# Kernel optimization log

Measured on AMD Instinct MI355X. Metric: run time of the kernel, lower is better.

## Reference

```python
import jax, jax.numpy as jnp
import numpy as np

NEG_SLOPE = 0.01  # torch F.leaky_relu default


def setup_inputs() -> dict:
    key = jax.random.key(0)
    k1, k2, k3, k4 = jax.random.split(key, 4)
    N, E, R, D = 100000, 1250000, 16, 64
    ego_embed = jax.random.normal(k1, (N, D), dtype=jnp.float32) * 0.1
    relation_weights = jax.random.normal(k2, (R, D, D), dtype=jnp.float32) * (1.0 / np.sqrt(D))
    edge_index = jax.random.randint(k3, (2, E), 0, N, dtype=jnp.int32)
    edge_type = jax.random.randint(k4, (E,), 0, R, dtype=jnp.int32)
    return {"ego_embed": ego_embed, "relation_weights": relation_weights,
            "edge_index": edge_index, "edge_type": edge_type}


def reference(ego_embed, relation_weights, edge_index, edge_type):
    head, tail = edge_index[0], edge_index[1]
    n_entities = ego_embed.shape[0]
    # Transform every node by every relation once ([R,N,D]) instead of
    # materializing the per-edge [E,D,D] weight gather the torch bmm implies;
    # same math: transformed_head[e] = ego_embed[head[e]] @ W[edge_type[e]].
    transformed_all = jnp.einsum('nd,rdk->rnk', ego_embed, relation_weights)
    transformed_head = transformed_all[edge_type, head]        # [E, D]
    tail_emb = ego_embed[tail]                                  # [E, D]
    scores = jax.nn.leaky_relu(jnp.sum(transformed_head * tail_emb, axis=1),
                               negative_slope=NEG_SLOPE)        # [E]
    exp_scores = jnp.exp(scores)                                # unnormalized attention
    denom = jax.ops.segment_sum(exp_scores, head, num_segments=n_entities)[head]
    norm_att = exp_scores / denom                               # segment softmax
    weighted = tail_emb * norm_att[:, None]                     # [E, D]
    # scatter_mean: segment sum / per-segment edge count (clamped to 1)
    summed = jax.ops.segment_sum(weighted, head, num_segments=n_entities)
    counts = jax.ops.segment_sum(jnp.ones_like(exp_scores), head, num_segments=n_entities)
    return summed / jnp.maximum(counts, 1.0)[:, None]
```

## Files before the change

kernel.cpp:

```cpp
#include <hip/hip_runtime.h>
#include <stdint.h>

#define NEG_SLOPE 0.01f
#define HPG 32
#define TSTR 72
#define BSH 5
#define NBMX 3200
#define K1CH 16384
#define CAP3 1024

typedef float f32x4 __attribute__((ext_vector_type(4)));
typedef short short8 __attribute__((ext_vector_type(8)));
typedef unsigned int u32;

#define DPPADD(v, ctrl) ((v) + __int_as_float(__builtin_amdgcn_update_dpp( \
        0, __float_as_int(v), (ctrl), 0xF, 0xF, true)))

__device__ inline short f2bf(float f) {
    union { float f; uint32_t u; } x; x.f = f;
    uint32_t r = x.u + 0x7FFF + ((x.u >> 16) & 1);
    return (short)(r >> 16);
}
__device__ inline float bf2f(unsigned short u) {
    union { uint32_t u; float f; } x; x.u = ((uint32_t)u) << 16; return x.f;
}

__global__ void __launch_bounds__(512) kA(
        const int* __restrict__ head, const int* __restrict__ tail,
        const int* __restrict__ etype, int E, int NB, int nblk,
        u32* __restrict__ staging, int* bucket_cur,
        const float* __restrict__ ego, unsigned short* __restrict__ ego_bf,
        int NE8, const float* __restrict__ rw, short* __restrict__ wfrag) {
    int t = threadIdx.x;
    int bid = blockIdx.x;
    if (bid < nblk) {
        __shared__ int lcnt[NBMX], lbase[NBMX], lfill[NBMX];
        for (int b = t; b < NBMX; b += 512) lcnt[b] = 0;
        __syncthreads();
        long long base = (long long)bid * K1CH;
        #pragma unroll
        for (int s = 0; s < K1CH / 512; ++s) {
            long long e = base + t + s * 512;
            if (e < E) atomicAdd(&lcnt[head[e] >> BSH], 1);
        }
        __syncthreads();
        for (int b = t; b < NB; b += 512) {
            int c = lcnt[b];
            lbase[b] = c ? atomicAdd(&bucket_cur[b], c) : 0;
            lfill[b] = 0;
        }
        __syncthreads();
        #pragma unroll
        for (int s = 0; s < K1CH / 512; ++s) {
            long long e = base + t + s * 512;
            if (e < E) {
                int h = head[e];
                int bk = h >> BSH;
                int rk = atomicAdd(&lfill[bk], 1);
                int pos = lbase[bk] + rk;
                if (pos >= CAP3) pos = CAP3 - 1;
                staging[(size_t)bk * CAP3 + pos] =
                    (u32)tail[e] | ((u32)etype[e] << 20) | ((u32)(h & 31) << 24);
            }
        }
    } else {
        int ib = bid - nblk;
        if (ib < 16) {
            int r = ib;
            int lane = t & 63;
            int c = lane & 15, q = lane >> 4;
            int pair = t >> 6;
            int t4 = pair >> 1, kh = pair & 1;
            int m = t4 * 16 + c;
            short8 f;
            for (int j = 0; j < 8; ++j) {
                int k = kh * 32 + q * 8 + j;
                f[j] = f2bf(rw[r * 4096 + k * 64 + m]);
            }
            *(short8*)(wfrag + ((size_t)((r * 4 + t4) * 2 + kh) * 64 + lane) * 8) = f;
        }
        int i = ib * 512 + t;
        if (i < NE8) {
            const float4* p = (const float4*)ego + (size_t)i * 2;
            float4 a = p[0], b = p[1];
            short8 v;
            v[0] = f2bf(a.x); v[1] = f2bf(a.y); v[2] = f2bf(a.z); v[3] = f2bf(a.w);
            v[4] = f2bf(b.x); v[5] = f2bf(b.y); v[6] = f2bf(b.z); v[7] = f2bf(b.w);
            *(short8*)(ego_bf + (size_t)i * 8) = v;
        }
    }
}

__global__ void __launch_bounds__(512, 4) k4_fused(
        const unsigned short* __restrict__ ego_bf,
        const short* __restrict__ wfrag,
        const u32* __restrict__ staging,
        const int* __restrict__ bucket_cur,
        float* __restrict__ out, int N) {
    __shared__ unsigned short T[16 * HPG * TSTR];
    __shared__ u32 lrec[CAP3];
    __shared__ int lhc[HPG], lofs[HPG], lcn[HPG];
    int tid = threadIdx.x;
    int wave = tid >> 6;
    int lane = tid & 63;
    int c = lane & 15, q = lane >> 4;
    int b = blockIdx.x;
    int hb = b * HPG;

    if (tid < HPG) lhc[tid] = 0;
    __syncthreads();
    int cnt_raw = bucket_cur[b];
    int cntb = cnt_raw > CAP3 ? CAP3 : cnt_raw;
    const u32* sb = staging + (size_t)b * CAP3;
    u32 r0 = 0, r1 = 0; int rk0 = -1, rk1 = -1;
    if (tid < cntb)       { r0 = sb[tid];       rk0 = atomicAdd(&lhc[r0 >> 24], 1); }
    if (tid + 512 < cntb) { r1 = sb[tid + 512]; rk1 = atomicAdd(&lhc[r1 >> 24], 1); }
    __syncthreads();
    if (tid < 64) {
        int v = (lane < HPG) ? lhc[lane] : 0;
        int inc = v;
        for (int off = 1; off < HPG; off <<= 1) {
            int u = __shfl_up(inc, off);
            if (lane >= off) inc += u;
        }
        if (lane < HPG) { lofs[lane] = inc - v; lcn[lane] = v; }
    }
    __syncthreads();
    if (rk0 >= 0) lrec[lofs[r0 >> 24] + rk0] = r0;
    if (rk1 >= 0) lrec[lofs[r1 >> 24] + rk1] = r1;

    for (int t = 0; t < 2; ++t) {
        int r = wave * 2 + t;
        const short* wp = wfrag + (size_t)r * 4096;
        short8 wf[4][2];
        #pragma unroll
        for (int t4 = 0; t4 < 4; ++t4)
            #pragma unroll
            for (int kh = 0; kh < 2; ++kh)
                wf[t4][kh] = *(const short8*)(wp + ((size_t)((t4 * 2 + kh) * 64 + lane)) * 8);
        #pragma unroll
        for (int hf = 0; hf < 2; ++hf) {
            int hrow = hb + hf * 16 + c;
            if (hrow >= N) hrow = N - 1;
            const unsigned short* hr = ego_bf + (size_t)hrow * 64;
            short8 b0 = *(const short8*)(hr + q * 8);
            short8 b1 = *(const short8*)(hr + 32 + q * 8);
            #pragma unroll
            for (int t4 = 0; t4 < 4; ++t4) {
                f32x4 a = {0.f, 0.f, 0.f, 0.f};
                a = __builtin_amdgcn_mfma_f32_16x16x32_bf16(wf[t4][0], b0, a, 0, 0, 0);
                a = __builtin_amdgcn_mfma_f32_16x16x32_bf16(wf[t4][1], b1, a, 0, 0, 0);
                ushort4 us;
                us.x = (unsigned short)f2bf(a[0]);
                us.y = (unsigned short)f2bf(a[1]);
                us.z = (unsigned short)f2bf(a[2]);
                us.w = (unsigned short)f2bf(a[3]);
                *(ushort4*)&T[(size_t)(r * HPG + hf * 16 + c) * TSTR + t4 * 16 + q * 4] = us;
            }
        }
    }
    __syncthreads();

    int hql = wave * 4 + q;
    int h = hb + hql;
    if (h >= N) return;
    int lq = c;
    int g2 = lq >> 3, c8 = lq & 7;
    int s0 = lofs[hql];
    int cnt = lcn[hql];
    int nbt = (cnt + 15) >> 4;
    float acc[8] = {0.f, 0.f, 0.f, 0.f, 0.f, 0.f, 0.f, 0.f};
    float den = 0.f;

    auto recAt = [&](int b2, int j) -> u32 {
        int idx = b2 * 16 + j * 2 + g2;
        return (idx < cnt) ? lrec[s0 + idx] : 0;
    };

    u32 rjA[8]; short8 rowsA[8];
    #pragma unroll
    for (int j = 0; j < 8; ++j) rjA[j] = recAt(0, j);
    #pragma unroll
    for (int j = 0; j < 8; ++j)
        rowsA[j] = *(const short8*)(ego_bf + (size_t)(rjA[j] & 0xFFFFF) * 64 + c8 * 8);
    for (int b2 = 0; b2 < nbt; ++b2) {
        u32 rjB[8]; short8 rowsB[8];
        bool more = (b2 + 1 < nbt);
        if (more) {
            #pragma unroll
            for (int j = 0; j < 8; ++j) rjB[j] = recAt(b2 + 1, j);
            #pragma unroll
            for (int j = 0; j < 8; ++j)
                rowsB[j] = *(const short8*)(ego_bf + (size_t)(rjB[j] & 0xFFFFF) * 64 + c8 * 8);
        }
        int ng = cnt - b2 * 16; if (ng > 16) ng = 16;
        #pragma unroll
        for (int sIt = 0; sIt < 8; ++sIt) {
            if (sIt * 2 < ng) {
                int ty = (rjA[sIt] >> 20) & 15;
                short8 trw = *(const short8*)&T[(size_t)(ty * HPG + hql) * TSTR + c8 * 8];
                float rf[8];
                float sa = 0.f, sb2 = 0.f;
                #pragma unroll
                for (int k = 0; k < 4; ++k) {
                    rf[k] = bf2f((unsigned short)rowsA[sIt][k]);
                    sa += rf[k] * bf2f((unsigned short)trw[k]);
                }
                #pragma unroll
                for (int k = 4; k < 8; ++k) {
                    rf[k] = bf2f((unsigned short)rowsA[sIt][k]);
                    sb2 += rf[k] * bf2f((unsigned short)trw[k]);
                }
                float s = sa + sb2;
                s = DPPADD(s, 0xB1);
                s = DPPADD(s, 0x4E);
                s = DPPADD(s, 0x141);
                float lr = s > 0.f ? s : NEG_SLOPE * s;
                float w = (sIt * 2 + g2 < ng) ? __expf(lr) : 0.f;
                den += w;
                #pragma unroll
                for (int k = 0; k < 8; ++k) acc[k] += w * rf[k];
            }
        }
        if (more) {
            #pragma unroll
            for (int j = 0; j < 8; ++j) { rjA[j] = rjB[j]; rowsA[j] = rowsB[j]; }
        }
    }
    den = DPPADD(den, 0x128);
    #pragma unroll
    for (int k = 0; k < 8; ++k) acc[k] = DPPADD(acc[k], 0x128);
    if (g2 == 0) {
        float sc = (cnt > 0) ? 1.f / (den * (float)cnt) : 0.f;
        float4 v0 = {acc[0] * sc, acc[1] * sc, acc[2] * sc, acc[3] * sc};
        float4 v1 = {acc[4] * sc, acc[5] * sc, acc[6] * sc, acc[7] * sc};
        float* op = out + (size_t)h * 64 + c8 * 8;
        *(float4*)op = v0;
        *(float4*)(op + 4) = v1;
    }
}

extern "C" void kernel_launch(void* const* d_in, const int* in_sizes, int n_in,
                              void* d_out, int out_size, void* d_ws, size_t ws_size,
                              hipStream_t stream) {
    const float* ego = (const float*)d_in[0];
    const float* rw  = (const float*)d_in[1];
    const int* eidx  = (const int*)d_in[2];
    const int* etyp  = (const int*)d_in[3];
    int N = in_sizes[0] / 64;
    int E = in_sizes[3];
    const int* head = eidx;
    const int* tail = eidx + E;
    float* out = (float*)d_out;

    char* ws = (char*)d_ws;
    size_t o = 0;
    auto take = [&](size_t bytes) -> char* {
        char* p = ws + o;
        o = (o + bytes + 255) & ~(size_t)255;
        return p;
    };
    int NB = (N + HPG - 1) >> BSH;
    if (NB > NBMX) NB = NBMX;
    int nblk = (E + K1CH - 1) / K1CH;
    int NE8 = N * 8;
    int nbI = (NE8 + 511) / 512;
    if (nbI < 16) nbI = 16;
    unsigned short* ego_bf = (unsigned short*)take((size_t)N * 64 * 2);
    short* wfrag    = (short*)take(16 * 4096 * 2);
    u32* staging    = (u32*)take((size_t)NB * CAP3 * 4);
    int* bucket_cur = (int*)take((size_t)NBMX * 4);
    (void)ws_size; (void)n_in; (void)out_size;

    hipMemsetAsync(bucket_cur, 0, (size_t)NBMX * 4, stream);
    kA<<<nblk + nbI, 512, 0, stream>>>(head, tail, etyp, E, NB, nblk,
                                       staging, bucket_cur,
                                       ego, ego_bf, NE8, rw, wfrag);
    k4_fused<<<NB, 512, 0, stream>>>(ego_bf, wfrag, staging, bucket_cur,
                                     out, N);
}
```

Before: 196.6 us.

## Fuse all stages into one cooperative persistent kernel with grid syncs

Replaces the memset plus two-kernel pipeline with a single cooperative-launch persistent kernel of 512 blocks, separated by grid-wide syncs: bf16 conversion, edge binning, then per-tile attention aggregation. Binning now uses coarse 256-head buckets with 4096-edge chunks, and each tile re-scans its coarse bucket to pick out its 32 heads. The aim is to remove launch and memset overhead and cut global atomic contention on bucket counters. In exchange, each coarse bucket's staging is read 8 times, grid syncs are added, and heads beyond per-tile capacity are truncated. It falls back to two regular kernels if cooperative launch is unavailable.

```diff
diff --git a/kernel.cpp b/kernel.cpp
--- a/kernel.cpp
+++ b/kernel.cpp
@@ -1,13 +1,17 @@
 #include <hip/hip_runtime.h>
+#include <hip/hip_cooperative_groups.h>
 #include <stdint.h>
+
+namespace cg = cooperative_groups;
 
 #define NEG_SLOPE 0.01f
 #define HPG 32
 #define TSTR 72
-#define BSH 5
-#define NBMX 3200
-#define K1CH 16384
+#define CAPC 4096
 #define CAP3 1024
+#define NBCMX 512
+#define CH 4096
+#define GRID 512
 
 typedef float f32x4 __attribute__((ext_vector_type(4)));
 typedef short short8 __attribute__((ext_vector_type(8)));
@@ -25,112 +29,114 @@
     union { uint32_t u; float f; } x; x.u = ((uint32_t)u) << 16; return x.f;
 }
 
-__global__ void __launch_bounds__(512) kA(
-        const int* __restrict__ head, const int* __restrict__ tail,
-        const int* __restrict__ etype, int E, int NB, int nblk,
-        u32* __restrict__ staging, int* bucket_cur,
+__device__ inline void dev_stage0(int bid, int t, int gsz, bool zero_cur,
+        int* bucket_cur, int nbc,
         const float* __restrict__ ego, unsigned short* __restrict__ ego_bf,
         int NE8, const float* __restrict__ rw, short* __restrict__ wfrag) {
-    int t = threadIdx.x;
-    int bid = blockIdx.x;
-    if (bid < nblk) {
-        __shared__ int lcnt[NBMX], lbase[NBMX], lfill[NBMX];
-        for (int b = t; b < NBMX; b += 512) lcnt[b] = 0;
-        __syncthreads();
-        long long base = (long long)bid * K1CH;
-        #pragma unroll
-        for (int s = 0; s < K1CH / 512; ++s) {
-            long long e = base + t + s * 512;
-            if (e < E) atomicAdd(&lcnt[head[e] >> BSH], 1);
-        }
-        __syncthreads();
-        for (int b = t; b < NB; b += 512) {
-            int c = lcnt[b];
-            lbase[b] = c ? atomicAdd(&bucket_cur[b], c) : 0;
-            lfill[b] = 0;
-        }
-        __syncthreads();
-        #pragma unroll
-        for (int s = 0; s < K1CH / 512; ++s) {
-            long long e = base + t + s * 512;
-            if (e < E) {
-                int h = head[e];
-                int bk = h >> BSH;
-                int rk = atomicAdd(&lfill[bk], 1);
-                int pos = lbase[bk] + rk;
-                if (pos >= CAP3) pos = CAP3 - 1;
-                staging[(size_t)bk * CAP3 + pos] =
-                    (u32)tail[e] | ((u32)etype[e] << 20) | ((u32)(h & 31) << 24);
-            }
-        }
-    } else {
-        int ib = bid - nblk;
-        if (ib < 16) {
-            int r = ib;
-            int lane = t & 63;
-            int c = lane & 15, q = lane >> 4;
-            int pair = t >> 6;
-            int t4 = pair >> 1, kh = pair & 1;
-            int m = t4 * 16 + c;
-            short8 f;
-            for (int j = 0; j < 8; ++j) {
-                int k = kh * 32 + q * 8 + j;
-                f[j] = f2bf(rw[r * 4096 + k * 64 + m]);
-            }
-            *(short8*)(wfrag + ((size_t)((r * 4 + t4) * 2 + kh) * 64 + lane) * 8) = f;
-        }
-        int i = ib * 512 + t;
-        if (i < NE8) {
-            const float4* p = (const float4*)ego + (size_t)i * 2;
-            float4 a = p[0], b = p[1];
-            short8 v;
-            v[0] = f2bf(a.x); v[1] = f2bf(a.y); v[2] = f2bf(a.z); v[3] = f2bf(a.w);
-            v[4] = f2bf(b.x); v[5] = f2bf(b.y); v[6] = f2bf(b.z); v[7] = f2bf(b.w);
-            *(short8*)(ego_bf + (size_t)i * 8) = v;
-        }
-    }
-}
-
-__global__ void __launch_bounds__(512, 4) k4_fused(
-        const unsigned short* __restrict__ ego_bf,
-        const short* __restrict__ wfrag,
-        const u32* __restrict__ staging,
-        const int* __restrict__ bucket_cur,
-        float* __restrict__ out, int N) {
-    __shared__ unsigned short T[16 * HPG * TSTR];
-    __shared__ u32 lrec[CAP3];
-    __shared__ int lhc[HPG], lofs[HPG], lcn[HPG];
-    int tid = threadIdx.x;
-    int wave = tid >> 6;
-    int lane = tid & 63;
-    int c = lane & 15, q = lane >> 4;
-    int b = blockIdx.x;
-    int hb = b * HPG;
-
-    if (tid < HPG) lhc[tid] = 0;
-    __syncthreads();
-    int cnt_raw = bucket_cur[b];
-    int cntb = cnt_raw > CAP3 ? CAP3 : cnt_raw;
-    const u32* sb = staging + (size_t)b * CAP3;
-    u32 r0 = 0, r1 = 0; int rk0 = -1, rk1 = -1;
-    if (tid < cntb)       { r0 = sb[tid];       rk0 = atomicAdd(&lhc[r0 >> 24], 1); }
-    if (tid + 512 < cntb) { r1 = sb[tid + 512]; rk1 = atomicAdd(&lhc[r1 >> 24], 1); }
-    __syncthreads();
-    if (tid < 64) {
-        int v = (lane < HPG) ? lhc[lane] : 0;
+    if (zero_cur && bid == 0 && t < nbc) bucket_cur[t] = 0;
+    if (bid >= 16 && bid < 32) {
+        int r = bid - 16;
+        int lane = t & 63;
+        int c = lane & 15, q = lane >> 4;
+        int pair = t >> 6;
+        int t4 = pair >> 1, kh = pair & 1;
+        int m = t4 * 16 + c;
+        short8 f;
+        for (int j = 0; j < 8; ++j) {
+            int k = kh * 32 + q * 8 + j;
+            f[j] = f2bf(rw[r * 4096 + k * 64 + m]);
+        }
+        *(short8*)(wfrag + ((size_t)((r * 4 + t4) * 2 + kh) * 64 + lane) * 8) = f;
+    }
+    for (int i = bid * 512 + t; i < NE8; i += gsz * 512) {
+        const float4* p = (const float4*)ego + (size_t)i * 2;
+        float4 a = p[0], b = p[1];
+        short8 v;
+        v[0] = f2bf(a.x); v[1] = f2bf(a.y); v[2] = f2bf(a.z); v[3] = f2bf(a.w);
+        v[4] = f2bf(b.x); v[5] = f2bf(b.y); v[6] = f2bf(b.z); v[7] = f2bf(b.w);
+        *(short8*)(ego_bf + (size_t)i * 8) = v;
+    }
+}
+
+__device__ inline void dev_bin(int ch, int t,
+        const int* __restrict__ head, const int* __restrict__ tail,
+        const int* __restrict__ etype, int E, int nbc,
+        u32* __restrict__ staging, int* bucket_cur,
+        int* lcnt, int* lbase, int* lfill) {
+    for (int b = t; b < NBCMX; b += 512) lcnt[b] = 0;
+    __syncthreads();
+    long long base = (long long)ch * CH;
+    #pragma unroll
+    for (int s = 0; s < CH / 512; ++s) {
+        long long e = base + t + s * 512;
+        if (e < E) atomicAdd(&lcnt[head[e] >> 8], 1);
+    }
+    __syncthreads();
+    for (int b = t; b < nbc; b += 512) {
+        int c = lcnt[b];
+        lbase[b] = c ? atomicAdd(&bucket_cur[b], c) : 0;
+        lfill[b] = 0;
+    }
+    __syncthreads();
+    #pragma unroll
+    for (int s = 0; s < CH / 512; ++s) {
+        long long e = base + t + s * 512;
+        if (e < E) {
+            int h = head[e];
+            int bk = h >> 8;
+            int rk = atomicAdd(&lfill[bk], 1);
+            int pos = lbase[bk] + rk;
+            if (pos >= CAPC) pos = CAPC - 1;
+            staging[(size_t)bk * CAPC + pos] =
+                (u32)tail[e] | ((u32)etype[e] << 20) | ((u32)(h & 255) << 24);
+        }
+    }
+    __syncthreads();
+}
+
+__device__ inline void dev_tile(int c, int s, int t, int N,
+        const unsigned short* __restrict__ ego_bf, const short* __restrict__ wfrag,
+        const u32* __restrict__ staging, const int* __restrict__ bucket_cur,
+        float* __restrict__ out,
+        unsigned short* T, u32* lrec, int* lhc, int* lofs, int* lcn, int* lfil) {
+    int wave = t >> 6;
+    int lane = t & 63;
+    int cc = lane & 15, q = lane >> 4;
+    int hb = c * 256 + s * 32;
+
+    __syncthreads();
+    if (t < 32) lhc[t] = 0;
+    __syncthreads();
+    int cnt_raw = bucket_cur[c];
+    int cntb = cnt_raw > CAPC ? CAPC : cnt_raw;
+    const u32* sbc = staging + (size_t)c * CAPC;
+    for (int t0 = t; t0 < cntb; t0 += 512) {
+        u32 rec = sbc[t0];
+        int hl = rec >> 24;
+        if ((hl >> 5) == s) atomicAdd(&lhc[hl & 31], 1);
+    }
+    __syncthreads();
+    if (t < 64) {
+        int v = (lane < 32) ? lhc[lane] : 0;
         int inc = v;
-        for (int off = 1; off < HPG; off <<= 1) {
+        for (int off = 1; off < 32; off <<= 1) {
             int u = __shfl_up(inc, off);
             if (lane >= off) inc += u;
         }
-        if (lane < HPG) { lofs[lane] = inc - v; lcn[lane] = v; }
-    }
-    __syncthreads();
-    if (rk0 >= 0) lrec[lofs[r0 >> 24] + rk0] = r0;
-    if (rk1 >= 0) lrec[lofs[r1 >> 24] + rk1] = r1;
-
-    for (int t = 0; t < 2; ++t) {
-        int r = wave * 2 + t;
+        if (lane < 32) { lofs[lane] = inc - v; lcn[lane] = v; lfil[lane] = inc - v; }
+    }
+    __syncthreads();
+    for (int t0 = t; t0 < cntb; t0 += 512) {
+        u32 rec = sbc[t0];
+        int hl = rec >> 24;
+        if ((hl >> 5) == s) {
+            int p2 = atomicAdd(&lfil[hl & 31], 1);
+            if (p2 < CAP3) lrec[p2] = rec;
+        }
+    }
+
+    for (int tt = 0; tt < 2; ++tt) {
+        int r = wave * 2 + tt;
         const short* wp = wfrag + (size_t)r * 4096;
         short8 wf[4][2];
         #pragma unroll
@@ -140,7 +146,7 @@
                 wf[t4][kh] = *(const short8*)(wp + ((size_t)((t4 * 2 + kh) * 64 + lane)) * 8);
         #pragma unroll
         for (int hf = 0; hf < 2; ++hf) {
-            int hrow = hb + hf * 16 + c;
+            int hrow = hb + hf * 16 + cc;
             if (hrow >= N) hrow = N - 1;
             const unsigned short* hr = ego_bf + (size_t)hrow * 64;
             short8 b0 = *(const short8*)(hr + q * 8);
@@ -155,7 +161,7 @@
                 us.y = (unsigned short)f2bf(a[1]);
                 us.z = (unsigned short)f2bf(a[2]);
                 us.w = (unsigned short)f2bf(a[3]);
-                *(ushort4*)&T[(size_t)(r * HPG + hf * 16 + c) * TSTR + t4 * 16 + q * 4] = us;
+                *(ushort4*)&T[(size_t)(r * HPG + hf * 16 + cc) * TSTR + t4 * 16 + q * 4] = us;
             }
         }
     }
@@ -163,80 +169,151 @@
 
     int hql = wave * 4 + q;
     int h = hb + hql;
-    if (h >= N) return;
-    int lq = c;
-    int g2 = lq >> 3, c8 = lq & 7;
-    int s0 = lofs[hql];
-    int cnt = lcn[hql];
-    int nbt = (cnt + 15) >> 4;
-    float acc[8] = {0.f, 0.f, 0.f, 0.f, 0.f, 0.f, 0.f, 0.f};
-    float den = 0.f;
-
-    auto recAt = [&](int b2, int j) -> u32 {
-        int idx = b2 * 16 + j * 2 + g2;
-        return (idx < cnt) ? lrec[s0 + idx] : 0;
-    };
-
-    u32 rjA[8]; short8 rowsA[8];
-    #pragma unroll
-    for (int j = 0; j < 8; ++j) rjA[j] = recAt(0, j);
-    #pragma unroll
-    for (int j = 0; j < 8; ++j)
-        rowsA[j] = *(const short8*)(ego_bf + (size_t)(rjA[j] & 0xFFFFF) * 64 + c8 * 8);
-    for (int b2 = 0; b2 < nbt; ++b2) {
-        u32 rjB[8]; short8 rowsB[8];
-        bool more = (b2 + 1 < nbt);
-        if (more) {
+    if (h < N) {
+        int lq = cc;
+        int g2 = lq >> 3, c8 = lq & 7;
+        int s0 = lofs[hql];
+        int cnt = lcn[hql];
+        int avail = CAP3 - s0; if (cnt > avail) cnt = avail;
+        int nbt = (cnt + 15) >> 4;
+        float acc[8] = {0.f, 0.f, 0.f, 0.f, 0.f, 0.f, 0.f, 0.f};
+        float den = 0.f;
+        auto recAt = [&](int b2, int j) -> u32 {
+            int idx = b2 * 16 + j * 2 + g2;
+            return (idx < cnt) ? lrec[s0 + idx] : 0;
+        };
+        u32 rjA[8]; short8 rowsA[8];
+        #pragma unroll
+        for (int j = 0; j < 8; ++j) rjA[j] = recAt(0, j);
+        #pragma unroll
+        for (int j = 0; j < 8; ++j)
+            rowsA[j] = *(const short8*)(ego_bf + (size_t)(rjA[j] & 0xFFFFF) * 64 + c8 * 8);
+        for (int b2 = 0; b2 < nbt; ++b2) {
+            u32 rjB[8]; short8 rowsB[8];
+            bool more = (b2 + 1 < nbt);
+            if (more) {
+                #pragma unroll
+                for (int j = 0; j < 8; ++j) rjB[j] = recAt(b2 + 1, j);
+                #pragma unroll
+                for (int j = 0; j < 8; ++j)
+                    rowsB[j] = *(const short8*)(ego_bf + (size_t)(rjB[j] & 0xFFFFF) * 64 + c8 * 8);
+            }
+            int ng = cnt - b2 * 16; if (ng > 16) ng = 16;
             #pragma unroll
-            for (int j = 0; j < 8; ++j) rjB[j] = recAt(b2 + 1, j);
-            #pragma unroll
-            for (int j = 0; j < 8; ++j)
-                rowsB[j] = *(const short8*)(ego_bf + (size_t)(rjB[j] & 0xFFFFF) * 64 + c8 * 8);
-        }
-        int ng = cnt - b2 * 16; if (ng > 16) ng = 16;
-        #pragma unroll
-        for (int sIt = 0; sIt < 8; ++sIt) {
-            if (sIt * 2 < ng) {
-                int ty = (rjA[sIt] >> 20) & 15;
-                short8 trw = *(const short8*)&T[(size_t)(ty * HPG + hql) * TSTR + c8 * 8];
-                float rf[8];
-                float sa = 0.f, sb2 = 0.f;
+            for (int sIt = 0; sIt < 8; ++sIt) {
+                if (sIt * 2 < ng) {
+                    int ty = (rjA[sIt] >> 20) & 15;
+                    short8 trw = *(const short8*)&T[(size_t)(ty * HPG + hql) * TSTR + c8 * 8];
+                    float rf[8];
+                    float sa = 0.f, sb2 = 0.f;
+                    #pragma unroll
+                    for (int k = 0; k < 4; ++k) {
+                        rf[k] = bf2f((unsigned short)rowsA[sIt][k]);
+                        sa += rf[k] * bf2f((unsigned short)trw[k]);
+                    }
+                    #pragma unroll
+                    for (int k = 4; k < 8; ++k) {
+                        rf[k] = bf2f((unsigned short)rowsA[sIt][k]);
+                        sb2 += rf[k] * bf2f((unsigned short)trw[k]);
+                    }
+                    float sv = sa + sb2;
+                    sv = DPPADD(sv, 0xB1);
+                    sv = DPPADD(sv, 0x4E);
+                    sv = DPPADD(sv, 0x141);
+                    float lr = sv > 0.f ? sv : NEG_SLOPE * sv;
+                    float w = (sIt * 2 + g2 < ng) ? __expf(lr) : 0.f;
+                    den += w;
+                    #pragma unroll
+                    for (int k = 0; k < 8; ++k) acc[k] += w * rf[k];
+                }
+            }
+            if (more) {
                 #pragma unroll
-                for (int k = 0; k < 4; ++k) {
-                    rf[k] = bf2f((unsigned short)rowsA[sIt][k]);
-                    sa += rf[k] * bf2f((unsigned short)trw[k]);
-                }
-                #pragma unroll
-                for (int k = 4; k < 8; ++k) {
-                    rf[k] = bf2f((unsigned short)rowsA[sIt][k]);
-                    sb2 += rf[k] * bf2f((unsigned short)trw[k]);
-                }
-                float s = sa + sb2;
-                s = DPPADD(s, 0xB1);
-                s = DPPADD(s, 0x4E);
-                s = DPPADD(s, 0x141);
-                float lr = s > 0.f ? s : NEG_SLOPE * s;
-                float w = (sIt * 2 + g2 < ng) ? __expf(lr) : 0.f;
-                den += w;
-                #pragma unroll
-                for (int k = 0; k < 8; ++k) acc[k] += w * rf[k];
+                for (int j = 0; j < 8; ++j) { rjA[j] = rjB[j]; rowsA[j] = rowsB[j]; }
             }
         }
-        if (more) {
-            #pragma unroll
-            for (int j = 0; j < 8; ++j) { rjA[j] = rjB[j]; rowsA[j] = rowsB[j]; }
-        }
-    }
-    den = DPPADD(den, 0x128);
-    #pragma unroll
-    for (int k = 0; k < 8; ++k) acc[k] = DPPADD(acc[k], 0x128);
-    if (g2 == 0) {
-        float sc = (cnt > 0) ? 1.f / (den * (float)cnt) : 0.f;
-        float4 v0 = {acc[0] * sc, acc[1] * sc, acc[2] * sc, acc[3] * sc};
-        float4 v1 = {acc[4] * sc, acc[5] * sc, acc[6] * sc, acc[7] * sc};
-        float* op = out + (size_t)h * 64 + c8 * 8;
-        *(float4*)op = v0;
-        *(float4*)(op + 4) = v1;
+        den = DPPADD(den, 0x128);
+        #pragma unroll
+        for (int k = 0; k < 8; ++k) acc[k] = DPPADD(acc[k], 0x128);
+        if (g2 == 0) {
+            float sc = (cnt > 0) ? 1.f / (den * (float)cnt) : 0.f;
+            float4 v0 = {acc[0] * sc, acc[1] * sc, acc[2] * sc, acc[3] * sc};
+            float4 v1 = {acc[4] * sc, acc[5] * sc, acc[6] * sc, acc[7] * sc};
+            float* op = out + (size_t)h * 64 + c8 * 8;
+            *(float4*)op = v0;
+            *(float4*)(op + 4) = v1;
+        }
+    }
+}
+
+__global__ void __launch_bounds__(512, 4) k_mega(
+        const int* __restrict__ head, const int* __restrict__ tail,
+        const int* __restrict__ etype, int E,
+        const float* __restrict__ ego, unsigned short* __restrict__ ego_bf,
+        int NE8, const float* __restrict__ rw, short* __restrict__ wfrag,
+        u32* __restrict__ staging, int* bucket_cur, float* __restrict__ out,
+        int N, int nbc, int nbcp8, int nchunk) {
+    __shared__ __align__(16) char smem[78336];
+    unsigned short* T = (unsigned short*)smem;
+    u32* lrec = (u32*)(smem + 73728);
+    int* lhc  = (int*)(smem + 77824);
+    int* lofs = (int*)(smem + 77952);
+    int* lcn  = (int*)(smem + 78080);
+    int* lfil = (int*)(smem + 78208);
+    int* lcnt  = (int*)smem;
+    int* lbase = (int*)(smem + 2048);
+    int* lfill = (int*)(smem + 4096);
+    int bid = blockIdx.x, t = threadIdx.x;
+    int gsz = (int)gridDim.x;
+
+    dev_stage0(bid, t, gsz, true, bucket_cur, nbc, ego, ego_bf, NE8, rw, wfrag);
+    cg::this_grid().sync();
+    for (int ch = bid; ch < nchunk; ch += gsz)
+        dev_bin(ch, t, head, tail, etype, E, nbc, staging, bucket_cur,
+                lcnt, lbase, lfill);
+    cg::this_grid().sync();
+    int r8 = bid & 7, b0 = bid >> 3, stride = gsz >> 3;
+    for (int i = b0; i < nbcp8; i += stride) {
+        int c = r8 + 8 * (i >> 3), s = i & 7;
+        if (c < nbc)
+            dev_tile(c, s, t, N, ego_bf, wfrag, staging, bucket_cur, out,
+                     T, lrec, lhc, lofs, lcn, lfil);
+    }
+}
+
+__global__ void __launch_bounds__(512) k_stage01(
+        const int* __restrict__ head, const int* __restrict__ tail,
+        const int* __restrict__ etype, int E,
+        const float* __restrict__ ego, unsigned short* __restrict__ ego_bf,
+        int NE8, const float* __restrict__ rw, short* __restrict__ wfrag,
+        u32* __restrict__ staging, int* bucket_cur, int nbc, int nchunk) {
+    __shared__ int lcnt[NBCMX], lbase[NBCMX], lfill[NBCMX];
+    int bid = blockIdx.x, t = threadIdx.x;
+    int gsz = (int)gridDim.x;
+    dev_stage0(bid, t, gsz, false, bucket_cur, nbc, ego, ego_bf, NE8, rw, wfrag);
+    for (int ch = bid; ch < nchunk; ch += gsz)
+        dev_bin(ch, t, head, tail, etype, E, nbc, staging, bucket_cur,
+                lcnt, lbase, lfill);
+}
+
+__global__ void __launch_bounds__(512, 4) k_stage2(
+        const unsigned short* __restrict__ ego_bf, const short* __restrict__ wfrag,
+        const u32* __restrict__ staging, const int* __restrict__ bucket_cur,
+        float* __restrict__ out, int N, int nbc, int nbcp8) {
+    __shared__ __align__(16) char smem[78336];
+    unsigned short* T = (unsigned short*)smem;
+    u32* lrec = (u32*)(smem + 73728);
+    int* lhc  = (int*)(smem + 77824);
+    int* lofs = (int*)(smem + 77952);
+    int* lcn  = (int*)(smem + 78080);
+    int* lfil = (int*)(smem + 78208);
+    int bid = blockIdx.x, t = threadIdx.x;
+    int r8 = bid & 7, b0 = bid >> 3, stride = (int)gridDim.x >> 3;
+    for (int i = b0; i < nbcp8; i += stride) {
+        int c = r8 + 8 * (i >> 3), s = i & 7;
+        if (c < nbc)
+            dev_tile(c, s, t, N, ego_bf, wfrag, staging, bucket_cur, out,
+                     T, lrec, lhc, lofs, lcn, lfil);
     }
 }
 
@@ -260,22 +337,41 @@
         o = (o + bytes + 255) & ~(size_t)255;
         return p;
     };
-    int NB = (N + HPG - 1) >> BSH;
-    if (NB > NBMX) NB = NBMX;
-    int nblk = (E + K1CH - 1) / K1CH;
+    int nbc = (N + 255) >> 8;
+    if (nbc > NBCMX) nbc = NBCMX;
+    int nbcp8 = (nbc + 7) & ~7;
+    int nchunk = (E + CH - 1) / CH;
     int NE8 = N * 8;
-    int nbI = (NE8 + 511) / 512;
-    if (nbI < 16) nbI = 16;
     unsigned short* ego_bf = (unsigned short*)take((size_t)N * 64 * 2);
     short* wfrag    = (short*)take(16 * 4096 * 2);
-    u32* staging    = (u32*)take((size_t)NB * CAP3 * 4);
-    int* bucket_cur = (int*)take((size_t)NBMX * 4);
+    u32* staging    = (u32*)take((size_t)NBCMX * CAPC * 4);
+    int* bucket_cur = (int*)take((size_t)NBCMX * 4);
     (void)ws_size; (void)n_in; (void)out_size;
 
-    hipMemsetAsync(bucket_cur, 0, (size_t)NBMX * 4, stream);
-    kA<<<nblk + nbI, 512, 0, stream>>>(head, tail, etyp, E, NB, nblk,
-                                       staging, bucket_cur,
-                                       ego, ego_bf, NE8, rw, wfrag);
-    k4_fused<<<NB, 512, 0, stream>>>(ego_bf, wfrag, staging, bucket_cur,
-                                     out, N);
-}
+    static int coop_state = -1;
+    if (coop_state < 0) {
+        int dev = 0;
+        hipGetDevice(&dev);
+        int v = 0;
+        hipDeviceGetAttribute(&v, hipDeviceAttributeCooperativeLaunch, dev);
+        coop_state = v ? 1 : 0;
+    }
+    if (coop_state == 1) {
+        void* args[] = {
+            (void*)&head, (void*)&tail, (void*)&etyp, (void*)&E,
+            (void*)&ego, (void*)&ego_bf, (void*)&NE8, (void*)&rw, (void*)&wfrag,
+            (void*)&staging, (void*)&bucket_cur, (void*)&out,
+            (void*)&N, (void*)&nbc, (void*)&nbcp8, (void*)&nchunk };
+        hipError_t err = hipLaunchCooperativeKernel(
+            (const void*)k_mega, dim3(GRID), dim3(512), args, 0, stream);
+        if (err != hipSuccess) coop_state = 0;
+    }
+    if (coop_state == 0) {
+        hipMemsetAsync(bucket_cur, 0, (size_t)NBCMX * 4, stream);
+        k_stage01<<<GRID, 512, 0, stream>>>(head, tail, etyp, E, ego, ego_bf,
+                                            NE8, rw, wfrag, staging, bucket_cur,
+                                            nbc, nchunk);
+        k_stage2<<<GRID, 512, 0, stream>>>(ego_bf, wfrag, staging, bucket_cur,
+                                           out, N, nbc, nbcp8);
+    }
+}
```

New measurement: 279.3 us. +42.1%, slower.
